# Kernel tuning notes

Hardware: AMD Instinct MI355X
Metric: run time of the kernel (lower is better)

## Reference

```python
import jax, jax.numpy as jnp
import numpy as np
import math

B, T, D_MODEL, H = 2, 2048, 768, 12
D = D_MODEL // H
EPS = 1e-8


def _l2norm(x, eps=EPS):
    # torch.nn.functional.normalize: x / max(||x||, eps)
    n = jnp.sqrt(jnp.sum(x * x, axis=-1, keepdims=True))
    return x / jnp.maximum(n, eps)


def setup_inputs() -> dict:
    key = jax.random.key(0)
    ks = jax.random.split(key, 7)
    sc = 1.0 / math.sqrt(D_MODEL)
    inp = {
        "query": jax.random.normal(ks[0], (B, T, D_MODEL), jnp.float32),
        "key": jax.random.normal(ks[1], (B, T, D_MODEL), jnp.float32),
        "value": jax.random.normal(ks[2], (B, T, D_MODEL), jnp.float32),
        "Wq": jax.random.normal(ks[3], (D_MODEL, D_MODEL), jnp.float32) * sc,
        "Wk": jax.random.normal(ks[4], (D_MODEL, D_MODEL), jnp.float32) * sc,
        "Wv": jax.random.normal(ks[5], (D_MODEL, D_MODEL), jnp.float32) * sc,
        "Wo": jax.random.normal(ks[6], (D_MODEL, D_MODEL), jnp.float32) * sc,
        "s_v": jnp.linspace(0.0, math.log(255.0), H).astype(jnp.float32),
        "s_r": jnp.zeros((H,), jnp.float32),
    }
    return inp


def reference(query, key, value, Wq, Wk, Wv, Wo, s_v, s_r):
    b, t, _ = query.shape

    def proj(x, W):  # Linear(bias=False) then split heads -> [B,H,T,D]
        return (x @ W.T).reshape(b, t, H, D).transpose(0, 2, 1, 3)

    q = _l2norm(proj(query, Wq))
    k = _l2norm(proj(key, Wk))
    v = _l2norm(proj(value, Wv))

    w = jnp.exp(s_v) + 1.0  # per-head decay exponent, in [2, 256]
    r = jnp.exp(s_r) + 1.0  # per-head scale

    # cosine-similarity scores in [-1, 1]
    s = jnp.einsum("bhqd,bhkd->bhqk", q, k)
    base = jnp.clip((s + 1.0) * 0.5, 0.0, 1.0)
    alpha = r[None, :, None, None] * jnp.power(base, w[None, :, None, None])

    # causal mask (no softmax normalization in screening attention)
    causal = jnp.tril(jnp.ones((t, t), dtype=bool))
    alpha = jnp.where(causal[None, None], alpha, 0.0)

    out = jnp.einsum("bhqk,bhkd->bhqd", alpha, v)  # [B,H,T,D]

    # TanhNorm: bound magnitude along head dim via tanh of the norm
    n = jnp.sqrt(jnp.sum(out * out, axis=-1, keepdims=True))
    out = jnp.tanh(n) * out / (n + EPS)

    out = out.transpose(0, 2, 1, 3).reshape(b, t, D_MODEL)
    return out @ Wo.T
```

## Files before the change

kernel.cpp:

```cpp
#include <hip/hip_runtime.h>
#include <hip/hip_bf16.h>
#include <math.h>


typedef __attribute__((ext_vector_type(8))) short short8;
typedef __attribute__((ext_vector_type(4))) float f32x4;
typedef __attribute__((ext_vector_type(4))) unsigned int uint4v;
typedef __attribute__((ext_vector_type(2))) unsigned int uint2v;
typedef __attribute__((ext_vector_type(4))) float float4v;

#define MFMA_BF16(a, b, c) __builtin_amdgcn_mfma_f32_16x16x32_bf16((a), (b), (c), 0, 0, 0)

static __device__ __forceinline__ unsigned short f2bf(float f) {
  union { float f; unsigned u; } v; v.f = f;
  unsigned r = v.u + 0x7FFFu + ((v.u >> 16) & 1u);
  return (unsigned short)(r >> 16);
}
static __device__ __forceinline__ unsigned pack2(float a, float b) {
  return (unsigned)f2bf(a) | ((unsigned)f2bf(b) << 16);
}
static __device__ __forceinline__ void gload_lds16(const void* g, void* l) {
  __builtin_amdgcn_global_load_lds((const __attribute__((address_space(1))) unsigned int*)g,
                                   (__attribute__((address_space(3))) unsigned int*)l, 16, 0, 0);
}

__global__ __launch_bounds__(256) void k_cvt(
    const float* __restrict__ s0, const float* __restrict__ s1, const float* __restrict__ s2,
    const float* __restrict__ s3, const float* __restrict__ s4, const float* __restrict__ s5,
    const float* __restrict__ s6, unsigned short* __restrict__ dst) {
  const size_t e = ((size_t)blockIdx.x * 256 + threadIdx.x) * 8;
  const float* src;
  size_t off;
  if (e < 9437184) {
    const int i = (int)(e / 3145728);
    src = (i == 0) ? s0 : (i == 1) ? s1 : s2;
    off = e - (size_t)i * 3145728;
  } else {
    const size_t ew = e - 9437184;
    const int i = (int)(ew / 589824);
    src = (i == 0) ? s3 : (i == 1) ? s4 : (i == 2) ? s5 : s6;
    off = ew - (size_t)i * 589824;
  }
  const float4v f0 = *(const float4v*)(src + off);
  const float4v f1 = *(const float4v*)(src + off + 4);
  uint4v u = {pack2(f0.x, f0.y), pack2(f0.z, f0.w), pack2(f1.x, f1.y), pack2(f1.z, f1.w)};
  *(uint4v*)(dst + e) = u;
}

__global__ __launch_bounds__(256) void k_proj(
    const unsigned short* __restrict__ Xb, const unsigned short* __restrict__ Wb,
    unsigned short* __restrict__ qb, unsigned short* __restrict__ kb,
    unsigned short* __restrict__ vtb) {
  __shared__ alignas(16) unsigned char smem[65536];
  float* o_s = (float*)smem;
  unsigned short* vt_s = (unsigned short*)smem;

  const int which = blockIdx.z;
  const unsigned short* X = Xb + (size_t)which * 3145728;
  const unsigned short* W = Wb + (size_t)which * 589824;

  const int mbase = blockIdx.x * 128;
  const int nb = blockIdx.y;
  const int tid = threadIdx.x;
  const int lane = tid & 63;
  const int wv = tid >> 6;
  const int wm = wv >> 1, wn = wv & 1;
  const int l15 = lane & 15, l4 = lane >> 4;

  const int srow8 = lane >> 3;
  const int schunk = (lane & 7) ^ srow8;

  f32x4 acc[4][4];
#pragma unroll
  for (int m = 0; m < 4; ++m)
#pragma unroll
    for (int n = 0; n < 4; ++n) acc[m][n] = (f32x4){0.f, 0.f, 0.f, 0.f};

#pragma unroll
  for (int i = 0; i < 4; ++i) {
    const int j = wv * 4 + i;
    gload_lds16(X + (size_t)(mbase + j * 8 + srow8) * 768 + schunk * 8, smem + j * 1024);
    gload_lds16(W + (size_t)(nb * 128 + j * 8 + srow8) * 768 + schunk * 8,
                smem + 16384 + j * 1024);
  }

  for (int ks = 0; ks < 12; ++ks) {
    const int cur = (ks & 1) * 32768;
    asm volatile("s_waitcnt vmcnt(0)" ::: "memory");
    __builtin_amdgcn_sched_barrier(0);
    __builtin_amdgcn_s_barrier();
    __builtin_amdgcn_sched_barrier(0);
    if (ks < 11) {
      const int nxt = ((ks + 1) & 1) * 32768;
      const int k0n = (ks + 1) * 64;
#pragma unroll
      for (int i = 0; i < 4; ++i) {
        const int j = wv * 4 + i;
        gload_lds16(X + (size_t)(mbase + j * 8 + srow8) * 768 + k0n + schunk * 8,
                    smem + nxt + j * 1024);
        gload_lds16(W + (size_t)(nb * 128 + j * 8 + srow8) * 768 + k0n + schunk * 8,
                    smem + nxt + 16384 + j * 1024);
      }
      __builtin_amdgcn_sched_barrier(0);
    }
    __builtin_amdgcn_s_setprio(1);
#pragma unroll
    for (int kc = 0; kc < 2; ++kc) {
      const int cx = (kc << 2) | l4;
      short8 ar[4], br[4];
#pragma unroll
      for (int m = 0; m < 4; ++m) {
        const int r = wm * 64 + m * 16 + l15;
        ar[m] = *(const short8*)(smem + cur + r * 128 + ((cx ^ (r & 7)) << 4));
      }
#pragma unroll
      for (int n = 0; n < 4; ++n) {
        const int r = wn * 64 + n * 16 + l15;
        br[n] = *(const short8*)(smem + cur + 16384 + r * 128 + ((cx ^ (r & 7)) << 4));
      }
#pragma unroll
      for (int m = 0; m < 4; ++m)
#pragma unroll
        for (int n = 0; n < 4; ++n) acc[m][n] = MFMA_BF16(ar[m], br[n], acc[m][n]);
    }
    __builtin_amdgcn_s_setprio(0);
  }

  const int b = mbase >> 11;
  const int tbase = mbase & 2047;
  const int row2 = tid >> 1, half = tid & 1;
  for (int p = 0; p < 2; ++p) {
    __syncthreads();
    if (wn == p) {
#pragma unroll
      for (int m = 0; m < 4; ++m)
#pragma unroll
        for (int n = 0; n < 4; ++n)
#pragma unroll
          for (int j = 0; j < 4; ++j)
            o_s[(wm * 64 + m * 16 + l4 * 4 + j) * 68 + n * 16 + l15] = acc[m][n][j];
    }
    __syncthreads();
    float v[32];
    float ss = 0.f;
#pragma unroll
    for (int c = 0; c < 8; ++c) {
      float4v f = *(const float4v*)(o_s + row2 * 68 + half * 32 + c * 4);
      v[c * 4 + 0] = f.x; v[c * 4 + 1] = f.y; v[c * 4 + 2] = f.z; v[c * 4 + 3] = f.w;
      ss += f.x * f.x + f.y * f.y + f.z * f.z + f.w * f.w;
    }
    ss += __shfl_xor(ss, 1);
    const float inv = 1.f / fmaxf(sqrtf(ss), 1e-8f);
    const int h = nb * 2 + p, bh = b * 12 + h;
    if (which < 2) {
      unsigned short* outp =
          ((which == 0) ? qb : kb) + ((size_t)bh * 2048 + tbase + row2) * 64 + half * 32;
#pragma unroll
      for (int c = 0; c < 4; ++c) {
        uint4v o = {pack2(v[c * 8 + 0] * inv, v[c * 8 + 1] * inv),
                    pack2(v[c * 8 + 2] * inv, v[c * 8 + 3] * inv),
                    pack2(v[c * 8 + 4] * inv, v[c * 8 + 5] * inv),
                    pack2(v[c * 8 + 6] * inv, v[c * 8 + 7] * inv)};
        *(uint4v*)(outp + c * 8) = o;
      }
      __syncthreads();
    } else {
      __syncthreads();
#pragma unroll
      for (int c = 0; c < 32; ++c)
        vt_s[(half * 32 + c) * 136 + row2] = f2bf(v[c] * inv);
      __syncthreads();
      const int d = tid >> 2, tc = (tid & 3) * 32;
      unsigned short* dst = vtb + ((size_t)bh * 64 + d) * 2048 + tbase + tc;
#pragma unroll
      for (int c = 0; c < 4; ++c)
        *(uint4v*)(dst + c * 8) = *(const uint4v*)(vt_s + d * 136 + tc + c * 8);
      __syncthreads();
    }
  }
}

__global__ __launch_bounds__(256) void k_attn(
    const unsigned short* __restrict__ qb, const unsigned short* __restrict__ kb,
    const unsigned short* __restrict__ vtb, const float* __restrict__ s_v,
    const float* __restrict__ s_r, unsigned short* __restrict__ attn) {
  __shared__ alignas(16) unsigned char smem[50176];
  unsigned short* p_s = (unsigned short*)(smem + 32768);
  float* o_s = (float*)smem;

  const int bid = blockIdx.x;
  const int ii = bid & 255, jj = bid >> 8;
  const int rank = (jj == 0) ? ii : (jj == 1) ? (511 - ii) : (512 + ii);
  const int qt = 31 - (rank / 24);
  const int bh = rank % 24;
  const int b = bh / 12, h = bh % 12;
  const int qbase = qt * 64;
  const unsigned short* Qp = qb + (size_t)bh * 2048 * 64;
  const unsigned short* Kp = kb + (size_t)bh * 2048 * 64;
  const unsigned short* VTp = vtb + (size_t)bh * 64 * 2048;

  const int tid = threadIdx.x;
  const int lane = tid & 63;
  const int wv = tid >> 6;
  const int wm = wv >> 1, wn = wv & 1;
  const int l15 = lane & 15, l4 = lane >> 4;
  const int srow8 = lane >> 3;
  const int schunk = (lane & 7) ^ srow8;

  const float w_h = expf(s_v[h]) + 1.0f;
  const float lr_h = log2f(expf(s_r[h]) + 1.0f);

#pragma unroll
  for (int i = 0; i < 2; ++i) {
    const int j = wv * 2 + i;
    gload_lds16(Qp + (size_t)(qbase + j * 8 + srow8) * 64 + schunk * 8, smem + 41984 + j * 1024);
  }
#pragma unroll
  for (int i = 0; i < 2; ++i) {
    const int j = wv * 2 + i;
    gload_lds16(Kp + (size_t)(j * 8 + srow8) * 64 + schunk * 8, smem + j * 1024);
    gload_lds16(VTp + (size_t)(j * 8 + srow8) * 2048 + schunk * 8, smem + 16384 + j * 1024);
  }
  asm volatile("s_waitcnt vmcnt(0)" ::: "memory");
  __builtin_amdgcn_sched_barrier(0);
  __builtin_amdgcn_s_barrier();
  __builtin_amdgcn_sched_barrier(0);

  short8 qf[2][2];
#pragma unroll
  for (int n = 0; n < 2; ++n)
#pragma unroll
    for (int kc = 0; kc < 2; ++kc) {
      const int r = wn * 32 + n * 16 + l15;
      const int cx = (kc << 2) | l4;
      qf[n][kc] = *(const short8*)(smem + 41984 + r * 128 + ((cx ^ (r & 7)) << 4));
    }

  f32x4 acc_o[2][2];
#pragma unroll
  for (int m = 0; m < 2; ++m)
#pragma unroll
    for (int n = 0; n < 2; ++n) acc_o[m][n] = (f32x4){0.f, 0.f, 0.f, 0.f};

  for (int kt = 0; kt <= qt; ++kt) {
    const int cur = (kt & 1) * 8192;
    asm volatile("s_waitcnt vmcnt(0)" ::: "memory");
    __builtin_amdgcn_sched_barrier(0);
    __builtin_amdgcn_s_barrier();
    __builtin_amdgcn_sched_barrier(0);
    if (kt < qt) {
      const int nxt = ((kt + 1) & 1) * 8192;
      const int kb2 = (kt + 1) * 64;
#pragma unroll
      for (int i = 0; i < 2; ++i) {
        const int j = wv * 2 + i;
        gload_lds16(Kp + (size_t)(kb2 + j * 8 + srow8) * 64 + schunk * 8, smem + nxt + j * 1024);
        gload_lds16(VTp + (size_t)(j * 8 + srow8) * 2048 + kb2 + schunk * 8,
                    smem + 16384 + nxt + j * 1024);
      }
      __builtin_amdgcn_sched_barrier(0);
    }
    f32x4 s_acc[2][2];
#pragma unroll
    for (int m = 0; m < 2; ++m)
#pragma unroll
      for (int n = 0; n < 2; ++n) s_acc[m][n] = (f32x4){0.f, 0.f, 0.f, 0.f};
    __builtin_amdgcn_s_setprio(1);
#pragma unroll
    for (int kc = 0; kc < 2; ++kc) {
      const int cx = (kc << 2) | l4;
      const int r0 = wm * 32 + l15, r1 = wm * 32 + 16 + l15;
      short8 a0 = *(const short8*)(smem + cur + r0 * 128 + ((cx ^ (r0 & 7)) << 4));
      short8 a1 = *(const short8*)(smem + cur + r1 * 128 + ((cx ^ (r1 & 7)) << 4));
      s_acc[0][0] = MFMA_BF16(a0, qf[0][kc], s_acc[0][0]);
      s_acc[0][1] = MFMA_BF16(a0, qf[1][kc], s_acc[0][1]);
      s_acc[1][0] = MFMA_BF16(a1, qf[0][kc], s_acc[1][0]);
      s_acc[1][1] = MFMA_BF16(a1, qf[1][kc], s_acc[1][1]);
    }
    __builtin_amdgcn_s_setprio(0);
    const bool diag = (kt == qt);
#pragma unroll
    for (int m = 0; m < 2; ++m)
#pragma unroll
      for (int n = 0; n < 2; ++n) {
        const int lkb = wm * 32 + m * 16 + l4 * 4;
        const int lq = wn * 32 + n * 16 + l15;
        float av[4];
#pragma unroll
        for (int t = 0; t < 4; ++t) {
          const float base = __builtin_amdgcn_fmed3f(fmaf(s_acc[m][n][t], 0.5f, 0.5f), 0.f, 1.f);
          float a = __builtin_amdgcn_exp2f(fmaf(w_h, __builtin_amdgcn_logf(base), lr_h));
          if (diag && (lkb + t) > lq) a = 0.f;
          av[t] = a;
        }
        uint2v u = {pack2(av[0], av[1]), pack2(av[2], av[3])};
        *(uint2v*)(p_s + lq * 72 + lkb) = u;
      }
    asm volatile("s_waitcnt lgkmcnt(0)" ::: "memory");
    __builtin_amdgcn_sched_barrier(0);
    __builtin_amdgcn_s_barrier();
    __builtin_amdgcn_sched_barrier(0);
    __builtin_amdgcn_s_setprio(1);
#pragma unroll
    for (int kc = 0; kc < 2; ++kc) {
      const int cx = (kc << 2) | l4;
      const int r0 = wm * 32 + l15, r1 = wm * 32 + 16 + l15;
      short8 pa0 = *(const short8*)(p_s + (wn * 32 + l15) * 72 + kc * 32 + l4 * 8);
      short8 pa1 = *(const short8*)(p_s + (wn * 32 + 16 + l15) * 72 + kc * 32 + l4 * 8);
      short8 vb0 = *(const short8*)(smem + 16384 + cur + r0 * 128 + ((cx ^ (r0 & 7)) << 4));
      short8 vb1 = *(const short8*)(smem + 16384 + cur + r1 * 128 + ((cx ^ (r1 & 7)) << 4));
      acc_o[0][0] = MFMA_BF16(pa0, vb0, acc_o[0][0]);
      acc_o[0][1] = MFMA_BF16(pa0, vb1, acc_o[0][1]);
      acc_o[1][0] = MFMA_BF16(pa1, vb0, acc_o[1][0]);
      acc_o[1][1] = MFMA_BF16(pa1, vb1, acc_o[1][1]);
    }
    __builtin_amdgcn_s_setprio(0);
  }
  __syncthreads();
#pragma unroll
  for (int qi = 0; qi < 2; ++qi)
#pragma unroll
    for (int di = 0; di < 2; ++di)
#pragma unroll
      for (int j = 0; j < 4; ++j)
        o_s[(wn * 32 + qi * 16 + l4 * 4 + j) * 68 + wm * 32 + di * 16 + l15] = acc_o[qi][di][j];
  __syncthreads();
  {
    const int row = tid >> 2, q4 = tid & 3;
    float vals[16];
    float ss = 0.f;
#pragma unroll
    for (int j = 0; j < 16; ++j) {
      vals[j] = o_s[row * 68 + q4 * 16 + j];
      ss += vals[j] * vals[j];
    }
    ss += __shfl_xor(ss, 1);
    ss += __shfl_xor(ss, 2);
    const float nrm = sqrtf(ss);
    const float sc = tanhf(nrm) / (nrm + 1e-8f);
    unsigned short* dst = attn + (size_t)(b * 2048 + qbase + row) * 768 + h * 64 + q4 * 16;
    uint4v o0 = {pack2(vals[0] * sc, vals[1] * sc), pack2(vals[2] * sc, vals[3] * sc),
                 pack2(vals[4] * sc, vals[5] * sc), pack2(vals[6] * sc, vals[7] * sc)};
    uint4v o1 = {pack2(vals[8] * sc, vals[9] * sc), pack2(vals[10] * sc, vals[11] * sc),
                 pack2(vals[12] * sc, vals[13] * sc), pack2(vals[14] * sc, vals[15] * sc)};
    *(uint4v*)(dst) = o0;
    *(uint4v*)(dst + 8) = o1;
  }
}

__global__ __launch_bounds__(256) void k_outproj(const unsigned short* __restrict__ attn,
                                                 const unsigned short* __restrict__ Wob,
                                                 float* __restrict__ out) {
  __shared__ alignas(16) unsigned char smem[65536];
  const int mbase = blockIdx.x * 128;
  const int nb = blockIdx.y;
  const int tid = threadIdx.x;
  const int lane = tid & 63;
  const int wv = tid >> 6;
  const int wm = wv >> 1, wn = wv & 1;
  const int l15 = lane & 15, l4 = lane >> 4;
  const int srow8 = lane >> 3;
  const int schunk = (lane & 7) ^ srow8;

  f32x4 acc[4][4];
#pragma unroll
  for (int m = 0; m < 4; ++m)
#pragma unroll
    for (int n = 0; n < 4; ++n) acc[m][n] = (f32x4){0.f, 0.f, 0.f, 0.f};

#pragma unroll
  for (int i = 0; i < 4; ++i) {
    const int j = wv * 4 + i;
    gload_lds16(attn + (size_t)(mbase + j * 8 + srow8) * 768 + schunk * 8, smem + j * 1024);
    gload_lds16(Wob + (size_t)(nb * 128 + j * 8 + srow8) * 768 + schunk * 8,
                smem + 16384 + j * 1024);
  }

  for (int ks = 0; ks < 12; ++ks) {
    const int cur = (ks & 1) * 32768;
    asm volatile("s_waitcnt vmcnt(0)" ::: "memory");
    __builtin_amdgcn_sched_barrier(0);
    __builtin_amdgcn_s_barrier();
    __builtin_amdgcn_sched_barrier(0);
    if (ks < 11) {
      const int nxt = ((ks + 1) & 1) * 32768;
      const int k0n = (ks + 1) * 64;
#pragma unroll
      for (int i = 0; i < 4; ++i) {
        const int j = wv * 4 + i;
        gload_lds16(attn + (size_t)(mbase + j * 8 + srow8) * 768 + k0n + schunk * 8,
                    smem + nxt + j * 1024);
        gload_lds16(Wob + (size_t)(nb * 128 + j * 8 + srow8) * 768 + k0n + schunk * 8,
                    smem + nxt + 16384 + j * 1024);
      }
      __builtin_amdgcn_sched_barrier(0);
    }
    __builtin_amdgcn_s_setprio(1);
#pragma unroll
    for (int kc = 0; kc < 2; ++kc) {
      const int cx = (kc << 2) | l4;
      short8 ar[4], br[4];
#pragma unroll
      for (int m = 0; m < 4; ++m) {
        const int r = wm * 64 + m * 16 + l15;
        ar[m] = *(const short8*)(smem + cur + r * 128 + ((cx ^ (r & 7)) << 4));
      }
#pragma unroll
      for (int n = 0; n < 4; ++n) {
        const int r = wn * 64 + n * 16 + l15;
        br[n] = *(const short8*)(smem + cur + 16384 + r * 128 + ((cx ^ (r & 7)) << 4));
      }
#pragma unroll
      for (int m = 0; m < 4; ++m)
#pragma unroll
        for (int n = 0; n < 4; ++n) acc[m][n] = MFMA_BF16(ar[m], br[n], acc[m][n]);
    }
    __builtin_amdgcn_s_setprio(0);
  }
#pragma unroll
  for (int m = 0; m < 4; ++m)
#pragma unroll
    for (int n = 0; n < 4; ++n)
#pragma unroll
      for (int j = 0; j < 4; ++j)
        out[(size_t)(mbase + wm * 64 + m * 16 + l4 * 4 + j) * 768 + nb * 128 + wn * 64 + n * 16 +
            l15] = acc[m][n][j];
}

extern "C" void kernel_launch(void* const* d_in, const int* in_sizes, int n_in, void* d_out,
                              int out_size, void* d_ws, size_t ws_size, hipStream_t stream) {
  (void)in_sizes;
  (void)n_in;
  (void)out_size;
  (void)ws_size;
  const float* query = (const float*)d_in[0];
  const float* key = (const float*)d_in[1];
  const float* value = (const float*)d_in[2];
  const float* Wq = (const float*)d_in[3];
  const float* Wk = (const float*)d_in[4];
  const float* Wv = (const float*)d_in[5];
  const float* Wo = (const float*)d_in[6];
  const float* s_v = (const float*)d_in[7];
  const float* s_r = (const float*)d_in[8];
  float* out = (float*)d_out;

  unsigned short* cvt = (unsigned short*)d_ws;
  unsigned short* Xb = cvt;
  unsigned short* Wb = cvt + 9437184;
  unsigned short* qb = cvt + 11796480;
  unsigned short* kb = qb + 3145728;
  unsigned short* vtb = kb + 3145728;
  unsigned short* attn = cvt;

  k_cvt<<<5760, 256, 0, stream>>>(query, key, value, Wq, Wk, Wv, Wo, cvt);
  k_proj<<<dim3(32, 6, 3), 256, 0, stream>>>(Xb, Wb, qb, kb, vtb);
  k_attn<<<dim3(768), 256, 0, stream>>>(qb, kb, vtb, s_v, s_r, attn);
  k_outproj<<<dim3(32, 6), 256, 0, stream>>>(attn, Wb + 3 * 589824, out);
}
```

Baseline: 90.38 us.

## Fuse fp32-to-bf16 activation conversion into the QKV projection GEMM

The QKV projection kernel now reads the fp32 activations directly from global memory into registers and converts them to bf16 in-loop, with the next k-slice loaded a step ahead. The separate conversion pass is reduced to weights only. This removes the write and re-read of a bf16 copy of the three activation tensors. The cost is that each block now re-reads fp32 activations at twice the byte width once per N-block (6x redundancy), plus extra register pressure and pack work inside the MFMA loop.

New measurement: 133.6 us. +47.8%, slower.

```diff
diff --git a/kernel.cpp b/kernel.cpp
--- a/kernel.cpp
+++ b/kernel.cpp
@@ -24,23 +24,13 @@
                                    (__attribute__((address_space(3))) unsigned int*)l, 16, 0, 0);
 }
 
-__global__ __launch_bounds__(256) void k_cvt(
-    const float* __restrict__ s0, const float* __restrict__ s1, const float* __restrict__ s2,
+__global__ __launch_bounds__(256) void k_cvtW(
     const float* __restrict__ s3, const float* __restrict__ s4, const float* __restrict__ s5,
     const float* __restrict__ s6, unsigned short* __restrict__ dst) {
   const size_t e = ((size_t)blockIdx.x * 256 + threadIdx.x) * 8;
-  const float* src;
-  size_t off;
-  if (e < 9437184) {
-    const int i = (int)(e / 3145728);
-    src = (i == 0) ? s0 : (i == 1) ? s1 : s2;
-    off = e - (size_t)i * 3145728;
-  } else {
-    const size_t ew = e - 9437184;
-    const int i = (int)(ew / 589824);
-    src = (i == 0) ? s3 : (i == 1) ? s4 : (i == 2) ? s5 : s6;
-    off = ew - (size_t)i * 589824;
-  }
+  const int i = (int)(e / 589824);
+  const float* src = (i == 0) ? s3 : (i == 1) ? s4 : (i == 2) ? s5 : s6;
+  const size_t off = e - (size_t)i * 589824;
   const float4v f0 = *(const float4v*)(src + off);
   const float4v f1 = *(const float4v*)(src + off + 4);
   uint4v u = {pack2(f0.x, f0.y), pack2(f0.z, f0.w), pack2(f1.x, f1.y), pack2(f1.z, f1.w)};
@@ -48,15 +38,15 @@
 }
 
 __global__ __launch_bounds__(256) void k_proj(
-    const unsigned short* __restrict__ Xb, const unsigned short* __restrict__ Wb,
-    unsigned short* __restrict__ qb, unsigned short* __restrict__ kb,
-    unsigned short* __restrict__ vtb) {
-  __shared__ alignas(16) unsigned char smem[65536];
+    const float* __restrict__ Xq, const float* __restrict__ Xk, const float* __restrict__ Xv,
+    const unsigned short* __restrict__ Wb, unsigned short* __restrict__ qb,
+    unsigned short* __restrict__ kb, unsigned short* __restrict__ vtb) {
+  __shared__ alignas(16) unsigned char smem[34816];
   float* o_s = (float*)smem;
   unsigned short* vt_s = (unsigned short*)smem;
 
   const int which = blockIdx.z;
-  const unsigned short* X = Xb + (size_t)which * 3145728;
+  const float* X = (which == 0) ? Xq : (which == 1) ? Xk : Xv;
   const unsigned short* W = Wb + (size_t)which * 589824;
 
   const int mbase = blockIdx.x * 128;
@@ -76,30 +66,59 @@
 #pragma unroll
     for (int n = 0; n < 4; ++n) acc[m][n] = (f32x4){0.f, 0.f, 0.f, 0.f};
 
+  const float* arow[4];
+#pragma unroll
+  for (int m = 0; m < 4; ++m)
+    arow[m] = X + (size_t)(mbase + wm * 64 + m * 16 + l15) * 768 + l4 * 8;
+
+  float4v af[4][2][2];
+
+#pragma unroll
+  for (int m = 0; m < 4; ++m)
+#pragma unroll
+    for (int kc = 0; kc < 2; ++kc)
+#pragma unroll
+      for (int hf = 0; hf < 2; ++hf)
+        af[m][kc][hf] = *(const float4v*)(arow[m] + kc * 32 + hf * 4);
 #pragma unroll
   for (int i = 0; i < 4; ++i) {
     const int j = wv * 4 + i;
-    gload_lds16(X + (size_t)(mbase + j * 8 + srow8) * 768 + schunk * 8, smem + j * 1024);
-    gload_lds16(W + (size_t)(nb * 128 + j * 8 + srow8) * 768 + schunk * 8,
-                smem + 16384 + j * 1024);
+    gload_lds16(W + (size_t)(nb * 128 + j * 8 + srow8) * 768 + schunk * 8, smem + j * 1024);
   }
 
   for (int ks = 0; ks < 12; ++ks) {
-    const int cur = (ks & 1) * 32768;
+    const int cur = (ks & 1) * 16384;
     asm volatile("s_waitcnt vmcnt(0)" ::: "memory");
     __builtin_amdgcn_sched_barrier(0);
     __builtin_amdgcn_s_barrier();
     __builtin_amdgcn_sched_barrier(0);
+    short8 afr[4][2];
+#pragma unroll
+    for (int m = 0; m < 4; ++m)
+#pragma unroll
+      for (int kc = 0; kc < 2; ++kc) {
+        union { uint4v u; short8 s; } cv;
+        cv.u = (uint4v){pack2(af[m][kc][0].x, af[m][kc][0].y),
+                        pack2(af[m][kc][0].z, af[m][kc][0].w),
+                        pack2(af[m][kc][1].x, af[m][kc][1].y),
+                        pack2(af[m][kc][1].z, af[m][kc][1].w)};
+        afr[m][kc] = cv.s;
+      }
     if (ks < 11) {
-      const int nxt = ((ks + 1) & 1) * 32768;
       const int k0n = (ks + 1) * 64;
+      const int nxt = ((ks + 1) & 1) * 16384;
+#pragma unroll
+      for (int m = 0; m < 4; ++m)
+#pragma unroll
+        for (int kc = 0; kc < 2; ++kc)
+#pragma unroll
+          for (int hf = 0; hf < 2; ++hf)
+            af[m][kc][hf] = *(const float4v*)(arow[m] + k0n + kc * 32 + hf * 4);
 #pragma unroll
       for (int i = 0; i < 4; ++i) {
         const int j = wv * 4 + i;
-        gload_lds16(X + (size_t)(mbase + j * 8 + srow8) * 768 + k0n + schunk * 8,
+        gload_lds16(W + (size_t)(nb * 128 + j * 8 + srow8) * 768 + k0n + schunk * 8,
                     smem + nxt + j * 1024);
-        gload_lds16(W + (size_t)(nb * 128 + j * 8 + srow8) * 768 + k0n + schunk * 8,
-                    smem + nxt + 16384 + j * 1024);
       }
       __builtin_amdgcn_sched_barrier(0);
     }
@@ -107,21 +126,16 @@
 #pragma unroll
     for (int kc = 0; kc < 2; ++kc) {
       const int cx = (kc << 2) | l4;
-      short8 ar[4], br[4];
-#pragma unroll
-      for (int m = 0; m < 4; ++m) {
-        const int r = wm * 64 + m * 16 + l15;
-        ar[m] = *(const short8*)(smem + cur + r * 128 + ((cx ^ (r & 7)) << 4));
-      }
+      short8 br[4];
 #pragma unroll
       for (int n = 0; n < 4; ++n) {
         const int r = wn * 64 + n * 16 + l15;
-        br[n] = *(const short8*)(smem + cur + 16384 + r * 128 + ((cx ^ (r & 7)) << 4));
+        br[n] = *(const short8*)(smem + cur + r * 128 + ((cx ^ (r & 7)) << 4));
       }
 #pragma unroll
       for (int m = 0; m < 4; ++m)
 #pragma unroll
-        for (int n = 0; n < 4; ++n) acc[m][n] = MFMA_BF16(ar[m], br[n], acc[m][n]);
+        for (int n = 0; n < 4; ++n) acc[m][n] = MFMA_BF16(afr[m][kc], br[n], acc[m][n]);
     }
     __builtin_amdgcn_s_setprio(0);
   }
@@ -444,16 +458,14 @@
   const float* s_r = (const float*)d_in[8];
   float* out = (float*)d_out;
 
-  unsigned short* cvt = (unsigned short*)d_ws;
-  unsigned short* Xb = cvt;
-  unsigned short* Wb = cvt + 9437184;
-  unsigned short* qb = cvt + 11796480;
+  unsigned short* Wb = (unsigned short*)d_ws;
+  unsigned short* qb = Wb + 2359296;
   unsigned short* kb = qb + 3145728;
   unsigned short* vtb = kb + 3145728;
-  unsigned short* attn = cvt;
-
-  k_cvt<<<5760, 256, 0, stream>>>(query, key, value, Wq, Wk, Wv, Wo, cvt);
-  k_proj<<<dim3(32, 6, 3), 256, 0, stream>>>(Xb, Wb, qb, kb, vtb);
+  unsigned short* attn = vtb + 3145728;
+
+  k_cvtW<<<1152, 256, 0, stream>>>(Wq, Wk, Wv, Wo, Wb);
+  k_proj<<<dim3(32, 6, 3), 256, 0, stream>>>(query, key, value, Wb, qb, kb, vtb);
   k_attn<<<dim3(768), 256, 0, stream>>>(qb, kb, vtb, s_v, s_r, attn);
   k_outproj<<<dim3(32, 6), 256, 0, stream>>>(attn, Wb + 3 * 589824, out);
 }
```
